# Optimization experiments

Hardware: AMD Instinct MI355X
Metric: run time of the kernel (lower is better)

## Reference

```python
import jax, jax.numpy as jnp
import numpy as np
import math

B, T, C, H = 4, 2048, 1024, 4
D = C // H
SCALE = 1.0 / math.sqrt(D)
EPS = 1e-5

def _cln(x, w, b):
    # channel-first LayerNorm over C of (B, C, T)
    mu = jnp.mean(x, axis=1, keepdims=True)
    r = x - mu
    s = jnp.mean(r * r, axis=1, keepdims=True)
    return r / jnp.sqrt(s + EPS) * w + b

def _dwconv(x, w, b=None):
    # depthwise conv1d: x (B, C, T), w (C, 1, 3), stride 1, pad 1
    y = jax.lax.conv_general_dilated(x, w, (1,), [(1, 1)], dimension_numbers=('NCH', 'OIH', 'NCH'), feature_group_count=x.shape[1])
    if b is not None:
        y = y + b[None, :, None]
    return y

def _conv1x1(x, w, b):
    # pointwise conv: x (B, C, T), w (Cout, Cin), b (Cout,)
    return jnp.einsum('oc,bct->bot', w, x) + b[None, :, None]

def _forward(x, mask, norm1_w, norm1_b, qconv_w, kconv_w, vconv_w, qnorm_w, qnorm_b, knorm_w, knorm_b, vnorm_w, vnorm_b, q1_w, q1_b, k1_w, k1_b, v1_w, v1_b, proj_w, proj_b, norm2_w, norm2_b, lin1_w, lin1_b, tc_w, tc_b, lin2_w, lin2_b):
    xc = jnp.swapaxes(x, 1, 2)                      # (B, C, T)
    h = _cln(xc, norm1_w, norm1_b)
    mf = mask.astype(x.dtype)                       # (B, 1, T); stride 1 -> interpolate is identity
    q = _conv1x1(_cln(_dwconv(h, qconv_w) * mf, qnorm_w, qnorm_b), q1_w, q1_b)
    k = _conv1x1(_cln(_dwconv(h, kconv_w) * mf, knorm_w, knorm_b), k1_w, k1_b)
    v = _conv1x1(_cln(_dwconv(h, vconv_w) * mf, vnorm_w, vnorm_b), v1_w, v1_b)
    # (B, H, T, D)
    q = jnp.swapaxes(q.reshape(B, H, D, T), 2, 3)
    k = jnp.swapaxes(k.reshape(B, H, D, T), 2, 3)
    v = jnp.swapaxes(v.reshape(B, H, D, T), 2, 3)
    att = jnp.einsum('bhqd,bhkd->bhqk', q * SCALE, k)
    att = jnp.where(mask[:, :, None, :], att, -jnp.inf)
    att = jax.nn.softmax(att, axis=-1)
    out = jnp.einsum('bhqk,bhkd->bhqd', att, v * mf[:, :, :, None])
    out = jnp.swapaxes(out, 2, 3).reshape(B, C, T)
    out = _conv1x1(out, proj_w, proj_b) * mf        # qx_mask == mask for stride 1
    x = x + jnp.swapaxes(out, 1, 2)                 # residual, (B, T, C)
    # Local_cnn branch
    h2 = jnp.swapaxes(_cln(jnp.swapaxes(x, 1, 2), norm2_w, norm2_b), 1, 2)  # (B, T, C)
    y = h2 @ lin1_w.T + lin1_b
    y = jnp.swapaxes(_dwconv(jnp.swapaxes(y, 1, 2), tc_w, tc_b), 1, 2)
    y = jax.nn.gelu(y, approximate=False)
    y = y @ lin2_w.T + lin2_b
    return x + y

def setup_inputs():
    key = jax.random.key(0)
    ks = jax.random.split(key, 16)
    f32 = jnp.float32
    x = jax.random.normal(ks[0], (B, T, C), dtype=f32)
    lengths = jax.random.randint(ks[1], (B,), T // 2, T + 1)
    mask = jnp.arange(T)[None, None, :] < lengths[:, None, None]  # (B, 1, T) bool
    dw_std = math.sqrt(2.0 / 3.0)
    px_std = math.sqrt(2.0 / C)
    d = dict(x=x, mask=mask)
    d['norm1_w'] = jnp.ones((1, C, 1), f32); d['norm1_b'] = jnp.zeros((1, C, 1), f32)
    d['qconv_w'] = jax.random.normal(ks[2], (C, 1, 3), dtype=f32) * dw_std
    d['kconv_w'] = jax.random.normal(ks[3], (C, 1, 3), dtype=f32) * dw_std
    d['vconv_w'] = jax.random.normal(ks[4], (C, 1, 3), dtype=f32) * dw_std
    for nm in ['qnorm', 'knorm', 'vnorm']:
        d[nm + '_w'] = jnp.ones((1, C, 1), f32); d[nm + '_b'] = jnp.zeros((1, C, 1), f32)
    d['q1_w'] = jax.random.normal(ks[5], (C, C), dtype=f32) * px_std; d['q1_b'] = jnp.zeros((C,), f32)
    d['k1_w'] = jax.random.normal(ks[6], (C, C), dtype=f32) * px_std; d['k1_b'] = jnp.zeros((C,), f32)
    d['v1_w'] = jax.random.normal(ks[7], (C, C), dtype=f32) * px_std; d['v1_b'] = jnp.zeros((C,), f32)
    d['proj_w'] = jax.random.normal(ks[8], (C, C), dtype=f32) * px_std; d['proj_b'] = jnp.zeros((C,), f32)
    d['norm2_w'] = jnp.ones((1, C, 1), f32); d['norm2_b'] = jnp.zeros((1, C, 1), f32)
    d['lin1_w'] = jax.random.normal(ks[9], (C, C), dtype=f32) * 0.02; d['lin1_b'] = jnp.zeros((C,), f32)
    d['tc_w'] = jax.random.normal(ks[10], (C, 1, 3), dtype=f32) * dw_std; d['tc_b'] = jnp.zeros((C,), f32)
    d['lin2_w'] = jax.random.normal(ks[11], (C, C), dtype=f32) * 0.02; d['lin2_b'] = jnp.zeros((C,), f32)
    return d

def reference(x, mask, norm1_w, norm1_b, qconv_w, kconv_w, vconv_w, qnorm_w, qnorm_b, knorm_w, knorm_b, vnorm_w, vnorm_b, q1_w, q1_b, k1_w, k1_b, v1_w, v1_b, proj_w, proj_b, norm2_w, norm2_b, lin1_w, lin1_b, tc_w, tc_b, lin2_w, lin2_b):
    return _forward(x, mask, norm1_w, norm1_b, qconv_w, kconv_w, vconv_w, qnorm_w, qnorm_b, knorm_w, knorm_b, vnorm_w, vnorm_b, q1_w, q1_b, k1_w, k1_b, v1_w, v1_b, proj_w, proj_b, norm2_w, norm2_b, lin1_w, lin1_b, tc_w, tc_b, lin2_w, lin2_b)
```

## Files before the change

### kernel.cpp

```cpp
#include <hip/hip_runtime.h>

#define BB 4
#define TT 2048
#define CC 1024
#define HH 4
#define DD 256
#define MM (BB*TT)

#define EPSV 1e-5f
#define NEGBIG (-1e30f)
#define SCALEV 0.0625f

typedef unsigned short u16;
typedef unsigned int   u32;
typedef __bf16 bf16x8 __attribute__((ext_vector_type(8)));
typedef float  f32x4  __attribute__((ext_vector_type(4)));

typedef u32 __attribute__((address_space(1))) gu32;
typedef u32 __attribute__((address_space(3))) lu32;

__device__ __forceinline__ u16 f2bf(float f){
  u32 u = __builtin_bit_cast(u32, f);
  u32 r = (u + 0x7fffu + ((u >> 16) & 1u)) >> 16;
  return (u16)r;
}
__device__ __forceinline__ float bf2f(u16 h){
  u32 u = ((u32)h) << 16;
  return __builtin_bit_cast(float, u);
}
__device__ __forceinline__ void gload_lds16(const u16* g, u16* l){
  __builtin_amdgcn_global_load_lds((const gu32*)g, (lu32*)l, 16, 0, 0);
}
__device__ __forceinline__ u32 cvtpk_bf16(float lo, float hi){
  u32 r;
  asm("v_cvt_pk_bf16_f32 %0, %1, %2" : "=v"(r) : "v"(lo), "v"(hi));
  return r;
}

__global__ __launch_bounds__(256) void conv_w_kernel(
    const float* __restrict__ w0, const float* __restrict__ w1, const float* __restrict__ w2,
    const float* __restrict__ w3, const float* __restrict__ w4, const float* __restrict__ w5,
    u16* __restrict__ o0, u16* __restrict__ o1, u16* __restrict__ o2,
    u16* __restrict__ o3, u16* __restrict__ o4, u16* __restrict__ o5){
  const int i = (blockIdx.x * 256 + threadIdx.x) * 4;
  const float* wsrc[6] = {w0,w1,w2,w3,w4,w5};
  u16* odst[6] = {o0,o1,o2,o3,o4,o5};
#pragma unroll
  for (int k = 0; k < 6; ++k){
    float4 v = *(const float4*)(wsrc[k] + i);
    ushort4 p; p.x=f2bf(v.x); p.y=f2bf(v.y); p.z=f2bf(v.z); p.w=f2bf(v.w);
    *(ushort4*)(odst[k] + i) = p;
  }
}

template<int OUTBF>
__global__ __launch_bounds__(256) void ln_rows(const float* __restrict__ x,
    const float* __restrict__ g, const float* __restrict__ be, void* __restrict__ out){
  const int row = blockIdx.x, tid = threadIdx.x;
  const float4 v = ((const float4*)(x + (size_t)row * CC))[tid];
  float s  = v.x + v.y + v.z + v.w;
  float ss = v.x*v.x + v.y*v.y + v.z*v.z + v.w*v.w;
  __shared__ float sb[8];
#pragma unroll
  for (int o = 1; o < 64; o <<= 1){ s += __shfl_xor(s, o); ss += __shfl_xor(ss, o); }
  const int wid = tid >> 6, lane = tid & 63;
  if (lane == 0){ sb[wid] = s; sb[4 + wid] = ss; }
  __syncthreads();
  s  = sb[0] + sb[1] + sb[2] + sb[3];
  ss = sb[4] + sb[5] + sb[6] + sb[7];
  const float mu = s * (1.0f / CC);
  const float rstd = rsqrtf(ss * (1.0f / CC) - mu * mu + EPSV);
  const float4 gg = ((const float4*)g)[tid];
  const float4 bb = ((const float4*)be)[tid];
  const float r0 = (v.x - mu) * rstd * gg.x + bb.x;
  const float r1 = (v.y - mu) * rstd * gg.y + bb.y;
  const float r2 = (v.z - mu) * rstd * gg.z + bb.z;
  const float r3 = (v.w - mu) * rstd * gg.w + bb.w;
  if (OUTBF){
    ushort4 p; p.x=f2bf(r0); p.y=f2bf(r1); p.z=f2bf(r2); p.w=f2bf(r3);
    *(ushort4*)((u16*)out + (size_t)row * CC + tid * 4) = p;
  } else {
    ((float4*)((float*)out + (size_t)row * CC))[tid] = make_float4(r0, r1, r2, r3);
  }
}

__global__ __launch_bounds__(256) void qkv_pre(const float* __restrict__ h,
    const int* __restrict__ mask,
    const float* __restrict__ qw, const float* __restrict__ kw, const float* __restrict__ vw,
    const float* __restrict__ qg, const float* __restrict__ qb2,
    const float* __restrict__ kg, const float* __restrict__ kb2,
    const float* __restrict__ vg, const float* __restrict__ vb2,
    u16* __restrict__ qn, u16* __restrict__ kn, u16* __restrict__ vn){
  const int row = blockIdx.x, tid = threadIdx.x;
  const int t = row & (TT - 1);
  const float mf = mask[row] ? 1.f : 0.f;
  const float4 z4 = make_float4(0.f, 0.f, 0.f, 0.f);
  const float4 x0 = ((const float4*)(h + (size_t)row * CC))[tid];
  const float4 xm = (t > 0)      ? ((const float4*)(h + (size_t)(row - 1) * CC))[tid] : z4;
  const float4 xp = (t < TT - 1) ? ((const float4*)(h + (size_t)(row + 1) * CC))[tid] : z4;
  const int c = tid * 4;
  const float am[4] = {xm.x, xm.y, xm.z, xm.w};
  const float a0[4] = {x0.x, x0.y, x0.z, x0.w};
  const float ap[4] = {xp.x, xp.y, xp.z, xp.w};
  float yq[4], yk[4], yv[4];
  float sq=0.f, ssq=0.f, sk=0.f, ssk=0.f, sv=0.f, ssv=0.f;
#pragma unroll
  for (int i = 0; i < 4; ++i){
    const float* qwp = qw + (c + i) * 3;
    const float* kwp = kw + (c + i) * 3;
    const float* vwp = vw + (c + i) * 3;
    const float q_ = (am[i]*qwp[0] + a0[i]*qwp[1] + ap[i]*qwp[2]) * mf;
    const float k_ = (am[i]*kwp[0] + a0[i]*kwp[1] + ap[i]*kwp[2]) * mf;
    const float v_ = (am[i]*vwp[0] + a0[i]*vwp[1] + ap[i]*vwp[2]) * mf;
    yq[i]=q_; yk[i]=k_; yv[i]=v_;
    sq+=q_; ssq+=q_*q_; sk+=k_; ssk+=k_*k_; sv+=v_; ssv+=v_*v_;
  }
  __shared__ float sb[24];
#pragma unroll
  for (int o = 1; o < 64; o <<= 1){
    sq += __shfl_xor(sq, o); ssq += __shfl_xor(ssq, o);
    sk += __shfl_xor(sk, o); ssk += __shfl_xor(ssk, o);
    sv += __shfl_xor(sv, o); ssv += __shfl_xor(ssv, o);
  }
  const int wid = tid >> 6, lane = tid & 63;
  if (lane == 0){
    sb[wid]=sq; sb[4+wid]=ssq; sb[8+wid]=sk; sb[12+wid]=ssk; sb[16+wid]=sv; sb[20+wid]=ssv;
  }
  __syncthreads();
  sq  = sb[0]+sb[1]+sb[2]+sb[3];    ssq = sb[4]+sb[5]+sb[6]+sb[7];
  sk  = sb[8]+sb[9]+sb[10]+sb[11];  ssk = sb[12]+sb[13]+sb[14]+sb[15];
  sv  = sb[16]+sb[17]+sb[18]+sb[19];ssv = sb[20]+sb[21]+sb[22]+sb[23];
  {
    const float mu = sq * (1.f/CC), rstd = rsqrtf(ssq*(1.f/CC) - mu*mu + EPSV);
    ushort4 p;
    p.x = f2bf((yq[0]-mu)*rstd*qg[c+0] + qb2[c+0]);
    p.y = f2bf((yq[1]-mu)*rstd*qg[c+1] + qb2[c+1]);
    p.z = f2bf((yq[2]-mu)*rstd*qg[c+2] + qb2[c+2]);
    p.w = f2bf((yq[3]-mu)*rstd*qg[c+3] + qb2[c+3]);
    *(ushort4*)(qn + (size_t)row * CC + c) = p;
  }
  {
    const float mu = sk * (1.f/CC), rstd = rsqrtf(ssk*(1.f/CC) - mu*mu + EPSV);
    ushort4 p;
    p.x = f2bf((yk[0]-mu)*rstd*kg[c+0] + kb2[c+0]);
    p.y = f2bf((yk[1]-mu)*rstd*kg[c+1] + kb2[c+1]);
    p.z = f2bf((yk[2]-mu)*rstd*kg[c+2] + kb2[c+2]);
    p.w = f2bf((yk[3]-mu)*rstd*kg[c+3] + kb2[c+3]);
    *(ushort4*)(kn + (size_t)row * CC + c) = p;
  }
  {
    const float mu = sv * (1.f/CC), rstd = rsqrtf(ssv*(1.f/CC) - mu*mu + EPSV);
    ushort4 p;
    p.x = f2bf((yv[0]-mu)*rstd*vg[c+0] + vb2[c+0]);
    p.y = f2bf((yv[1]-mu)*rstd*vg[c+1] + vb2[c+1]);
    p.z = f2bf((yv[2]-mu)*rstd*vg[c+2] + vb2[c+2]);
    p.w = f2bf((yv[3]-mu)*rstd*vg[c+3] + vb2[c+3]);
    *(ushort4*)(vn + (size_t)row * CC + c) = p;
  }
}

template<int MODE>
__global__ __launch_bounds__(256) void gemm_bt(
    const u16* __restrict__ A, const u16* __restrict__ Bw,
    const float* __restrict__ bias, void* __restrict__ out,
    const float* __restrict__ resid, const int* __restrict__ mask){
  __shared__ u16 As[128 * 32];
  __shared__ u16 Bs[128 * 32];
  const int tid = threadIdx.x, lane = tid & 63, wid = tid >> 6;
  const int wr = wid >> 1, wc = wid & 1;
  const int bm = blockIdx.x, bn = blockIdx.y;
  f32x4 acc[4][4];
#pragma unroll
  for (int i = 0; i < 4; ++i)
#pragma unroll
    for (int j = 0; j < 4; ++j) acc[i][j] = (f32x4){0.f, 0.f, 0.f, 0.f};
  const u16* gA = A  + (size_t)(bm * 128 + wid * 32 + (lane >> 2)) * CC + (lane & 3) * 8;
  const u16* gB = Bw + (size_t)(bn * 128 + wid * 32 + (lane >> 2)) * CC + (lane & 3) * 8;
  u16* lA = &As[wid * 1024];
  u16* lB = &Bs[wid * 1024];
  const int la = lane & 15, lg8 = (lane >> 4) * 8;
  for (int kt = 0; kt < CC / 32; ++kt){
    gload_lds16(gA + kt * 32, lA);
    gload_lds16(gA + kt * 32 + (size_t)16 * CC, lA + 512);
    gload_lds16(gB + kt * 32, lB);
    gload_lds16(gB + kt * 32 + (size_t)16 * CC, lB + 512);
    __syncthreads();
    bf16x8 af[4], bf[4];
#pragma unroll
    for (int mi = 0; mi < 4; ++mi) af[mi] = *(const bf16x8*)&As[(wr*64 + mi*16 + la)*32 + lg8];
#pragma unroll
    for (int ni = 0; ni < 4; ++ni) bf[ni] = *(const bf16x8*)&Bs[(wc*64 + ni*16 + la)*32 + lg8];
#pragma unroll
    for (int mi = 0; mi < 4; ++mi)
#pragma unroll
      for (int ni = 0; ni < 4; ++ni)
        acc[mi][ni] = __builtin_amdgcn_mfma_f32_16x16x32_bf16(af[mi], bf[ni], acc[mi][ni], 0, 0, 0);
    __syncthreads();
  }
  const int lg = lane >> 4;
#pragma unroll
  for (int mi = 0; mi < 4; ++mi){
    const int mb = bm * 128 + wr * 64 + mi * 16 + lg * 4;
#pragma unroll
    for (int ni = 0; ni < 4; ++ni){
      const int n = bn * 128 + wc * 64 + ni * 16 + la;
      const float bz = bias[n];
      if (MODE == 0){
        u16* o = (u16*)out;
#pragma unroll
        for (int j = 0; j < 4; ++j) o[(size_t)(mb + j) * CC + n] = f2bf(acc[mi][ni][j] + bz);
      } else if (MODE == 1){
        float* o = (float*)out;
#pragma unroll
        for (int j = 0; j < 4; ++j){
          const int m = mb + j;
          const float mf = mask[m] ? 1.f : 0.f;
          o[(size_t)m * CC + n] = (acc[mi][ni][j] + bz) * mf + resid[(size_t)m * CC + n];
        }
      } else if (MODE == 2){
        float* o = (float*)out;
#pragma unroll
        for (int j = 0; j < 4; ++j){
          const int m = mb + j;
          o[(size_t)m * CC + n] = acc[mi][ni][j] + bz + resid[(size_t)m * CC + n];
        }
      } else {
        u16* o = (u16*)out;
        const int bq = mb >> 11, tq = mb & (TT - 1);
        const int hq = n >> 8, dq = n & 255;
        ushort4 p;
        p.x = f2bf(acc[mi][ni][0] + bz); p.y = f2bf(acc[mi][ni][1] + bz);
        p.z = f2bf(acc[mi][ni][2] + bz); p.w = f2bf(acc[mi][ni][3] + bz);
        *(ushort4*)&o[(size_t)((bq * HH + hq) * DD + dq) * TT + tq] = p;
      }
    }
  }
}

__global__ __launch_bounds__(256, 3) void flash_attn(
    const u16* __restrict__ Q, const u16* __restrict__ Kg,
    const u16* __restrict__ Vt, const int* __restrict__ mask,
    u16* __restrict__ Oa){
  __shared__ __align__(16) u16 Ks[32 * 256];
  __shared__ __align__(16) u16 Vs[256 * 32];
  __shared__ __align__(16) u16 Ps[4][16 * 32];
  const int Dn = blockIdx.x;
  const int xcd = Dn & 7, idx = Dn >> 3;
  const int bh = xcd * 2 + (idx >> 5), qt = idx & 31;
  const int b = bh >> 2, h2 = bh & 3;
  const int tid = threadIdx.x, lane = tid & 63, wid = tid >> 6;
  const int la = lane & 15, lg = lane >> 4;

  const int* mrow = mask + b * TT;
  int len = 1024;
  {
    unsigned long long bal = __ballot(mrow[1024 + lane * 16] != 0);
    int ones = __popcll(bal);
    if (ones > 0){
      int lo = 1024 + (ones - 1) * 16;
      unsigned long long bal2 = __ballot(mrow[lo + la] != 0);
      len = lo + __popcll(bal2 & 0xFFFFull);
    }
  }
  const int nkt = (len + 31) >> 5;

  bf16x8 qf[8];
  const u16* qrow = Q + (size_t)(b * TT + qt * 64 + wid * 16 + la) * CC + h2 * DD + lg * 8;
#pragma unroll
  for (int kd = 0; kd < 8; ++kd) qf[kd] = *(const bf16x8*)(qrow + kd * 32);

  f32x4 oacc[16];
#pragma unroll
  for (int i = 0; i < 16; ++i) oacc[i] = (f32x4){0.f, 0.f, 0.f, 0.f};
  float mrun = NEGBIG, lrun = 0.f;

  const int krow = tid >> 5;
  const int kc = (tid & 31) ^ (krow & 7);
  const u16* ksrc = Kg + (size_t)(b * TT + krow) * CC + h2 * DD + kc * 8;
  const int vc = (tid & 3) ^ ((tid >> 3) & 3);
  const u16* vsrcb = Vt + (size_t)(bh * DD + (tid >> 2)) * TT + vc * 8;

#define STAGE_K(KT) { _Pragma("unroll") \
  for (int i = 0; i < 4; ++i) \
    gload_lds16(ksrc + (size_t)((KT) * 32 + i * 8) * CC, Ks + i * 2048 + tid * 8); }
#define STAGE_V(KT) { _Pragma("unroll") \
  for (int i = 0; i < 4; ++i) \
    gload_lds16(vsrcb + (size_t)(i * 64) * TT + (KT) * 32, Vs + i * 2048 + tid * 8); }

  STAGE_K(0); STAGE_V(0);
  __syncthreads();

  const char* KsB = (const char*)Ks;
  const char* VsB = (const char*)Vs;
  char* PsB = (char*)&Ps[wid][0];
  const int swk = (la & 7) << 4;
  const int swv = (la >> 1) & 3;
  const float sc2 = SCALEV * 1.44269504f;

  for (int kt = 0; kt < nkt; ++kt){
    f32x4 sfr[2];
#pragma unroll
    for (int fn = 0; fn < 2; ++fn){
      f32x4 s = (f32x4){0.f, 0.f, 0.f, 0.f};
      const int rk = fn * 16 + la;
#pragma unroll
      for (int kd = 0; kd < 8; ++kd){
        bf16x8 kf = *(const bf16x8*)(KsB + rk * 512 + ((kd * 64 + lg * 16) ^ swk));
        s = __builtin_amdgcn_mfma_f32_16x16x32_bf16(kf, qf[kd], s, 0, 0, 0);
      }
      sfr[fn] = s;
    }
    if (kt * 32 + 32 <= len){
      sfr[0] *= sc2; sfr[1] *= sc2;
    } else {
      const int kb = kt * 32 + lg * 4;
#pragma unroll
      for (int fn = 0; fn < 2; ++fn)
#pragma unroll
        for (int j = 0; j < 4; ++j)
          sfr[fn][j] = (kb + fn * 16 + j < len) ? sfr[fn][j] * sc2 : NEGBIG;
    }
    float tm = fmaxf(fmaxf(fmaxf(sfr[0][0], sfr[0][1]), fmaxf(sfr[0][2], sfr[0][3])),
                     fmaxf(fmaxf(sfr[1][0], sfr[1][1]), fmaxf(sfr[1][2], sfr[1][3])));
    tm = fmaxf(tm, __shfl_xor(tm, 16));
    tm = fmaxf(tm, __shfl_xor(tm, 32));
    if (!__all(tm <= mrun + 12.0f)){
      const float mn = fmaxf(mrun, tm);
      const float al = __builtin_exp2f(mrun - mn);
      mrun = mn; lrun *= al;
#pragma unroll
      for (int i = 0; i < 16; ++i) oacc[i] *= al;
    }
    float p0 = __builtin_exp2f(sfr[0][0] - mrun), p1 = __builtin_exp2f(sfr[0][1] - mrun);
    float p2 = __builtin_exp2f(sfr[0][2] - mrun), p3 = __builtin_exp2f(sfr[0][3] - mrun);
    float p4 = __builtin_exp2f(sfr[1][0] - mrun), p5 = __builtin_exp2f(sfr[1][1] - mrun);
    float p6 = __builtin_exp2f(sfr[1][2] - mrun), p7 = __builtin_exp2f(sfr[1][3] - mrun);
    float ts = ((p0 + p1) + (p2 + p3)) + ((p4 + p5) + (p6 + p7));
    ts += __shfl_xor(ts, 16);
    ts += __shfl_xor(ts, 32);
    lrun += ts;
    {
      uint2 w0; w0.x = cvtpk_bf16(p0, p1); w0.y = cvtpk_bf16(p2, p3);
      uint2 w1; w1.x = cvtpk_bf16(p4, p5); w1.y = cvtpk_bf16(p6, p7);
      char* pr = PsB + la * 64 + ((lg & 1) << 3);
      *(uint2*)(pr + ((((lg >> 1)    ) ^ swv) << 4)) = w0;
      *(uint2*)(pr + (((2 + (lg >> 1)) ^ swv) << 4)) = w1;
    }
    __syncthreads();
    if (kt + 1 < nkt) STAGE_K(kt + 1);
    bf16x8 pf = *(const bf16x8*)(PsB + la * 64 + ((lg ^ swv) << 4));
#pragma unroll
    for (int mi = 0; mi < 16; ++mi){
      bf16x8 vf = *(const bf16x8*)(VsB + (mi * 16 + la) * 64 + ((lg ^ swv) << 4));
      oacc[mi] = __builtin_amdgcn_mfma_f32_16x16x32_bf16(vf, pf, oacc[mi], 0, 0, 0);
    }
    __syncthreads();
    if (kt + 1 < nkt) STAGE_V(kt + 1);
  }
  const float inv = 1.f / lrun;
  u16* orow = Oa + (size_t)(b * TT + qt * 64 + wid * 16 + la) * CC + h2 * DD + lg * 4;
#pragma unroll
  for (int mi = 0; mi < 16; ++mi){
    ushort4 p;
    p.x = f2bf(oacc[mi][0] * inv); p.y = f2bf(oacc[mi][1] * inv);
    p.z = f2bf(oacc[mi][2] * inv); p.w = f2bf(oacc[mi][3] * inv);
    *(ushort4*)(orow + mi * 16) = p;
  }
#undef STAGE_K
#undef STAGE_V
}

__global__ __launch_bounds__(256) void tc_gelu(const u16* __restrict__ y2,
    const float* __restrict__ w, const float* __restrict__ bias, u16* __restrict__ y3){
  const int row = blockIdx.x, tid = threadIdx.x;
  const int t = row & (TT - 1);
  const int c = tid * 4;
  ushort4 z4; z4.x = z4.y = z4.z = z4.w = 0;
  const ushort4 u0 = *(const ushort4*)(y2 + (size_t)row * CC + c);
  const ushort4 um = (t > 0)      ? *(const ushort4*)(y2 + (size_t)(row - 1) * CC + c) : z4;
  const ushort4 up = (t < TT - 1) ? *(const ushort4*)(y2 + (size_t)(row + 1) * CC + c) : z4;
  const float am[4] = {bf2f(um.x), bf2f(um.y), bf2f(um.z), bf2f(um.w)};
  const float a0[4] = {bf2f(u0.x), bf2f(u0.y), bf2f(u0.z), bf2f(u0.w)};
  const float ap[4] = {bf2f(up.x), bf2f(up.y), bf2f(up.z), bf2f(up.w)};
  u16 pv[4];
#pragma unroll
  for (int i = 0; i < 4; ++i){
    const float* wp = w + (c + i) * 3;
    const float yv = am[i] * wp[0] + a0[i] * wp[1] + ap[i] * wp[2] + bias[c + i];
    const float ge = 0.5f * yv * (1.f + erff(yv * 0.7071067811865475f));
    pv[i] = f2bf(ge);
  }
  ushort4 p; p.x = pv[0]; p.y = pv[1]; p.z = pv[2]; p.w = pv[3];
  *(ushort4*)(y3 + (size_t)row * CC + c) = p;
}

extern "C" void kernel_launch(void* const* d_in, const int* in_sizes, int n_in,
                              void* d_out, int out_size, void* d_ws, size_t ws_size,
                              hipStream_t stream){
  const float* x     = (const float*)d_in[0];
  const int*   mask  = (const int*)d_in[1];
  const float* n1g   = (const float*)d_in[2];
  const float* n1b   = (const float*)d_in[3];
  const float* qconv = (const float*)d_in[4];
  const float* kconv = (const float*)d_in[5];
  const float* vconv = (const float*)d_in[6];
  const float* qg    = (const float*)d_in[7];
  const float* qbe   = (const float*)d_in[8];
  const float* kg    = (const float*)d_in[9];
  const float* kbe   = (const float*)d_in[10];
  const float* vg    = (const float*)d_in[11];
  const float* vbe   = (const float*)d_in[12];
  const float* q1w   = (const float*)d_in[13];
  const float* q1b   = (const float*)d_in[14];
  const float* k1w   = (const float*)d_in[15];
  const float* k1b   = (const float*)d_in[16];
  const float* v1w   = (const float*)d_in[17];
  const float* v1b   = (const float*)d_in[18];
  const float* pw    = (const float*)d_in[19];
  const float* pb    = (const float*)d_in[20];
  const float* n2g   = (const float*)d_in[21];
  const float* n2b   = (const float*)d_in[22];
  const float* l1w   = (const float*)d_in[23];
  const float* l1b   = (const float*)d_in[24];
  const float* tcw   = (const float*)d_in[25];
  const float* tcb   = (const float*)d_in[26];
  const float* l2w   = (const float*)d_in[27];
  const float* l2b   = (const float*)d_in[28];
  (void)in_sizes; (void)n_in; (void)out_size; (void)ws_size;

  char* ws = (char*)d_ws;
  const size_t MB = (size_t)1 << 20;
  u16* wq  = (u16*)(ws + 0 * MB);
  u16* wk  = (u16*)(ws + 2 * MB);
  u16* wv  = (u16*)(ws + 4 * MB);
  u16* wp2 = (u16*)(ws + 6 * MB);
  u16* wl1 = (u16*)(ws + 8 * MB);
  u16* wl2 = (u16*)(ws + 10 * MB);
  float* hbuf = (float*)(ws + 12 * MB);
  float* x2   = hbuf;
  u16* qn  = (u16*)(ws + 44 * MB);
  u16* kn  = (u16*)(ws + 60 * MB);
  u16* vn  = (u16*)(ws + 76 * MB);
  u16* Qb  = (u16*)(ws + 92 * MB);
  u16* Kb  = (u16*)(ws + 108 * MB);
  u16* Vtb = (u16*)(ws + 124 * MB);
  u16* AO  = qn;
  u16* y1  = kn;
  u16* y2  = vn;
  u16* y3  = Qb;

  conv_w_kernel<<<1024, 256, 0, stream>>>(q1w, k1w, v1w, pw, l1w, l2w, wq, wk, wv, wp2, wl1, wl2);
  ln_rows<0><<<MM, 256, 0, stream>>>(x, n1g, n1b, hbuf);
  qkv_pre<<<MM, 256, 0, stream>>>(hbuf, mask, qconv, kconv, vconv,
                                  qg, qbe, kg, kbe, vg, vbe, qn, kn, vn);
  gemm_bt<0><<<dim3(64, 8), 256, 0, stream>>>(qn, wq, q1b, Qb, nullptr, nullptr);
  gemm_bt<0><<<dim3(64, 8), 256, 0, stream>>>(kn, wk, k1b, Kb, nullptr, nullptr);
  gemm_bt<3><<<dim3(64, 8), 256, 0, stream>>>(vn, wv, v1b, Vtb, nullptr, nullptr);
  flash_attn<<<512, 256, 0, stream>>>(Qb, Kb, Vtb, mask, AO);
  gemm_bt<1><<<dim3(64, 8), 256, 0, stream>>>(AO, wp2, pb, x2, x, mask);
  ln_rows<1><<<MM, 256, 0, stream>>>(x2, n2g, n2b, y1);
  gemm_bt<0><<<dim3(64, 8), 256, 0, stream>>>(y1, wl1, l1b, y2, nullptr, nullptr);
  tc_gelu<<<MM, 256, 0, stream>>>(y2, tcw, tcb, y3);
  gemm_bt<2><<<dim3(64, 8), 256, 0, stream>>>(y3, wl2, l2b, (float*)d_out, x2, nullptr);
}
```

Before: 370.0 us.

## Deepen GEMM K-tile to 64 with XOR-swizzled LDS and batch QKV GEMMs

The shared GEMM core now stages 64-wide K tiles instead of 32. Each stage uses an XOR-swizzled LDS layout, which halves the number of barriers per K loop and avoids bank conflicts on the fragment reads. The three Q/K/V projection GEMMs are merged into one launch using blockIdx.z, which gives a 1536-block grid instead of three 512-block launches. In exchange, each block uses twice the LDS, which may lower occupancy, and the QKV kernel adds per-block pointer selection.

```diff
diff --git a/kernel.cpp b/kernel.cpp
--- a/kernel.cpp
+++ b/kernel.cpp
@@ -159,13 +159,52 @@
   }
 }
 
+__device__ __forceinline__ void gemm_core(const u16* __restrict__ A, const u16* __restrict__ Bw,
+    u16* As, u16* Bs, f32x4 acc[4][4], int bm, int bn, int tid){
+  const int lane = tid & 63, wid = tid >> 6;
+  const int wr = wid >> 1, wc = wid & 1;
+  const int la = lane & 15, lg = lane >> 4;
+  const int srow = tid >> 3;
+  const int schunk = (tid & 7) ^ (srow & 7);
+  const u16* gA = A  + (size_t)(bm * 128 + srow) * CC + schunk * 8;
+  const u16* gB = Bw + (size_t)(bn * 128 + srow) * CC + schunk * 8;
+  u16* dA = As + tid * 8;
+  u16* dB = Bs + tid * 8;
+  const int swz = (la & 7) << 4;
+  for (int kt = 0; kt < CC / 64; ++kt){
+#pragma unroll
+    for (int i = 0; i < 4; ++i){
+      gload_lds16(gA + (size_t)(i * 32) * CC + kt * 64, dA + i * 2048);
+      gload_lds16(gB + (size_t)(i * 32) * CC + kt * 64, dB + i * 2048);
+    }
+    __syncthreads();
+#pragma unroll
+    for (int kk = 0; kk < 2; ++kk){
+      bf16x8 af[4], bf[4];
+      const int co = (kk * 64 + lg * 16) ^ swz;
+#pragma unroll
+      for (int mi = 0; mi < 4; ++mi)
+        af[mi] = *(const bf16x8*)((const char*)As + (wr * 64 + mi * 16 + la) * 128 + co);
+#pragma unroll
+      for (int ni = 0; ni < 4; ++ni)
+        bf[ni] = *(const bf16x8*)((const char*)Bs + (wc * 64 + ni * 16 + la) * 128 + co);
+#pragma unroll
+      for (int mi = 0; mi < 4; ++mi)
+#pragma unroll
+        for (int ni = 0; ni < 4; ++ni)
+          acc[mi][ni] = __builtin_amdgcn_mfma_f32_16x16x32_bf16(af[mi], bf[ni], acc[mi][ni], 0, 0, 0);
+    }
+    __syncthreads();
+  }
+}
+
 template<int MODE>
 __global__ __launch_bounds__(256) void gemm_bt(
     const u16* __restrict__ A, const u16* __restrict__ Bw,
     const float* __restrict__ bias, void* __restrict__ out,
     const float* __restrict__ resid, const int* __restrict__ mask){
-  __shared__ u16 As[128 * 32];
-  __shared__ u16 Bs[128 * 32];
+  __shared__ __align__(16) u16 As[128 * 64];
+  __shared__ __align__(16) u16 Bs[128 * 64];
   const int tid = threadIdx.x, lane = tid & 63, wid = tid >> 6;
   const int wr = wid >> 1, wc = wid & 1;
   const int bm = blockIdx.x, bn = blockIdx.y;
@@ -174,30 +213,8 @@
   for (int i = 0; i < 4; ++i)
 #pragma unroll
     for (int j = 0; j < 4; ++j) acc[i][j] = (f32x4){0.f, 0.f, 0.f, 0.f};
-  const u16* gA = A  + (size_t)(bm * 128 + wid * 32 + (lane >> 2)) * CC + (lane & 3) * 8;
-  const u16* gB = Bw + (size_t)(bn * 128 + wid * 32 + (lane >> 2)) * CC + (lane & 3) * 8;
-  u16* lA = &As[wid * 1024];
-  u16* lB = &Bs[wid * 1024];
-  const int la = lane & 15, lg8 = (lane >> 4) * 8;
-  for (int kt = 0; kt < CC / 32; ++kt){
-    gload_lds16(gA + kt * 32, lA);
-    gload_lds16(gA + kt * 32 + (size_t)16 * CC, lA + 512);
-    gload_lds16(gB + kt * 32, lB);
-    gload_lds16(gB + kt * 32 + (size_t)16 * CC, lB + 512);
-    __syncthreads();
-    bf16x8 af[4], bf[4];
-#pragma unroll
-    for (int mi = 0; mi < 4; ++mi) af[mi] = *(const bf16x8*)&As[(wr*64 + mi*16 + la)*32 + lg8];
-#pragma unroll
-    for (int ni = 0; ni < 4; ++ni) bf[ni] = *(const bf16x8*)&Bs[(wc*64 + ni*16 + la)*32 + lg8];
-#pragma unroll
-    for (int mi = 0; mi < 4; ++mi)
-#pragma unroll
-      for (int ni = 0; ni < 4; ++ni)
-        acc[mi][ni] = __builtin_amdgcn_mfma_f32_16x16x32_bf16(af[mi], bf[ni], acc[mi][ni], 0, 0, 0);
-    __syncthreads();
-  }
-  const int lg = lane >> 4;
+  gemm_core(A, Bw, As, Bs, acc, bm, bn, tid);
+  const int la = lane & 15, lg = lane >> 4;
 #pragma unroll
   for (int mi = 0; mi < 4; ++mi){
     const int mb = bm * 128 + wr * 64 + mi * 16 + lg * 4;
@@ -217,21 +234,57 @@
           const float mf = mask[m] ? 1.f : 0.f;
           o[(size_t)m * CC + n] = (acc[mi][ni][j] + bz) * mf + resid[(size_t)m * CC + n];
         }
-      } else if (MODE == 2){
+      } else {
         float* o = (float*)out;
 #pragma unroll
         for (int j = 0; j < 4; ++j){
           const int m = mb + j;
           o[(size_t)m * CC + n] = acc[mi][ni][j] + bz + resid[(size_t)m * CC + n];
         }
+      }
+    }
+  }
+}
+
+__global__ __launch_bounds__(256) void gemm_qkv(
+    const u16* __restrict__ qn, const u16* __restrict__ kn, const u16* __restrict__ vn,
+    const u16* __restrict__ wq, const u16* __restrict__ wk, const u16* __restrict__ wv,
+    const float* __restrict__ qb, const float* __restrict__ kb, const float* __restrict__ vb,
+    u16* __restrict__ Qb, u16* __restrict__ Kb, u16* __restrict__ Vtb){
+  __shared__ __align__(16) u16 As[128 * 64];
+  __shared__ __align__(16) u16 Bs[128 * 64];
+  const int z = blockIdx.z;
+  const u16* A  = (z == 0) ? qn : (z == 1) ? kn : vn;
+  const u16* Bw = (z == 0) ? wq : (z == 1) ? wk : wv;
+  const float* bias = (z == 0) ? qb : (z == 1) ? kb : vb;
+  const int tid = threadIdx.x, lane = tid & 63, wid = tid >> 6;
+  const int wr = wid >> 1, wc = wid & 1;
+  const int bm = blockIdx.x, bn = blockIdx.y;
+  f32x4 acc[4][4];
+#pragma unroll
+  for (int i = 0; i < 4; ++i)
+#pragma unroll
+    for (int j = 0; j < 4; ++j) acc[i][j] = (f32x4){0.f, 0.f, 0.f, 0.f};
+  gemm_core(A, Bw, As, Bs, acc, bm, bn, tid);
+  const int la = lane & 15, lg = lane >> 4;
+#pragma unroll
+  for (int mi = 0; mi < 4; ++mi){
+    const int mb = bm * 128 + wr * 64 + mi * 16 + lg * 4;
+#pragma unroll
+    for (int ni = 0; ni < 4; ++ni){
+      const int n = bn * 128 + wc * 64 + ni * 16 + la;
+      const float bz = bias[n];
+      if (z < 2){
+        u16* o = z ? Kb : Qb;
+#pragma unroll
+        for (int j = 0; j < 4; ++j) o[(size_t)(mb + j) * CC + n] = f2bf(acc[mi][ni][j] + bz);
       } else {
-        u16* o = (u16*)out;
         const int bq = mb >> 11, tq = mb & (TT - 1);
         const int hq = n >> 8, dq = n & 255;
         ushort4 p;
         p.x = f2bf(acc[mi][ni][0] + bz); p.y = f2bf(acc[mi][ni][1] + bz);
         p.z = f2bf(acc[mi][ni][2] + bz); p.w = f2bf(acc[mi][ni][3] + bz);
-        *(ushort4*)&o[(size_t)((bq * HH + hq) * DD + dq) * TT + tq] = p;
+        *(ushort4*)&Vtb[(size_t)((bq * HH + hq) * DD + dq) * TT + tq] = p;
       }
     }
   }
@@ -453,9 +506,7 @@
   ln_rows<0><<<MM, 256, 0, stream>>>(x, n1g, n1b, hbuf);
   qkv_pre<<<MM, 256, 0, stream>>>(hbuf, mask, qconv, kconv, vconv,
                                   qg, qbe, kg, kbe, vg, vbe, qn, kn, vn);
-  gemm_bt<0><<<dim3(64, 8), 256, 0, stream>>>(qn, wq, q1b, Qb, nullptr, nullptr);
-  gemm_bt<0><<<dim3(64, 8), 256, 0, stream>>>(kn, wk, k1b, Kb, nullptr, nullptr);
-  gemm_bt<3><<<dim3(64, 8), 256, 0, stream>>>(vn, wv, v1b, Vtb, nullptr, nullptr);
+  gemm_qkv<<<dim3(64, 8, 3), 256, 0, stream>>>(qn, kn, vn, wq, wk, wv, q1b, k1b, v1b, Qb, Kb, Vtb);
   flash_attn<<<512, 256, 0, stream>>>(Qb, Kb, Vtb, mask, AO);
   gemm_bt<1><<<dim3(64, 8), 256, 0, stream>>>(AO, wp2, pb, x2, x, mask);
   ln_rows<1><<<MM, 256, 0, stream>>>(x2, n2g, n2b, y1);
```

Measured after the change: 355.9 us. 1.04x faster.
